# Kernel tuning notes

Hardware: AMD Instinct MI355X
Metric: run time of the kernel (lower is better)

## Reference

```python
import jax, jax.numpy as jnp
import numpy as np

B, IN_DIM, K, OUT_DIM = 512, 16384, 32, 16
DIMS = [8192, 4096, 2048]  # floor(dim/factor) per layer, factor=2


def setup_inputs() -> dict:
    key = jax.random.key(0)
    ks = jax.random.split(key, 16)
    inp = {"x": jax.random.normal(ks[0], (B, IN_DIM), dtype=jnp.float32)}
    prev = IN_DIM
    std = (2.0 / K) ** 0.5
    for i, d in enumerate(DIMS):
        inp[f"w{i}"] = jax.random.normal(ks[1 + i], (d, K), dtype=jnp.float32) * std
        inp[f"b{i}"] = jnp.zeros((1, d), dtype=jnp.float32)
        inp[f"knn{i}"] = jax.random.randint(ks[8 + i], (d, K), 0, prev, dtype=jnp.int64)
        prev = d
    inp["fc_w"] = jax.random.normal(ks[12], (DIMS[-1], OUT_DIM), dtype=jnp.float32) * (1.0 / DIMS[-1] ** 0.5)
    inp["fc_b"] = jnp.zeros((OUT_DIM,), dtype=jnp.float32)
    return inp


def reference(x, w0, b0, w1, b1, w2, b2, fc_w, fc_b, knn0, knn1, knn2):
    # Each layer: gather K neighbors per output unit, weighted sum over K, bias, ReLU.
    for w, b, knn in ((w0, b0, knn0), (w1, b1, knn1), (w2, b2, knn2)):
        g = x[:, knn]                              # (B, dim_i, K) irregular gather
        x = jax.nn.relu(jnp.einsum('bdk,dk->bd', g, w) + b)
    return x @ fc_w + fc_b                         # fc_angle
```

## Files before the change

### kernel.cpp

```cpp
#include <hip/hip_runtime.h>
#include <hip/hip_fp16.h>

#define BATCH   512
#define IN_DIM  16384
#define KNN     32

typedef __attribute__((ext_vector_type(4))) _Float16 half4v;

#define N0 (8192 * KNN)
#define N1 (4096 * KNN)
#define N2 (2048 * KNN)

__global__ __launch_bounds__(256) void prep_k(const int* __restrict__ k0,
                                              const float* __restrict__ w0,
                                              const int* __restrict__ k1,
                                              const float* __restrict__ w1,
                                              const int* __restrict__ k2,
                                              const float* __restrict__ w2,
                                              unsigned int* __restrict__ po) {
    const int t = blockIdx.x * 256 + threadIdx.x;
    int idx; float wv;
    if (t < N0) {
        idx = k0[t];            wv = w0[t];
    } else if (t < N0 + N1) {
        idx = k1[t - N0];       wv = w1[t - N0];
    } else if (t < N0 + N1 + N2) {
        idx = k2[t - N0 - N1];  wv = w2[t - N0 - N1];
    } else {
        return;
    }
    const unsigned short hb =
        __builtin_bit_cast(unsigned short, (_Float16)wv);
    po[t] = (unsigned int)(unsigned short)idx | ((unsigned int)hb << 16);
}

__global__ __launch_bounds__(256) void transpose_h(const float* __restrict__ in,
                                                   _Float16* __restrict__ out) {
    __shared__ float tile[32][33];
    const int bx = blockIdx.x * 32;
    const int by = blockIdx.y * 32;
    const int tx = threadIdx.x & 31;
    const int ty = threadIdx.x >> 5;
#pragma unroll
    for (int j = 0; j < 32; j += 8)
        tile[ty + j][tx] = in[(size_t)(by + ty + j) * IN_DIM + bx + tx];
    __syncthreads();
    const int r = threadIdx.x >> 3;
    const int c = (threadIdx.x & 7) * 4;
    half4v h;
    h[0] = (_Float16)tile[c + 0][r];
    h[1] = (_Float16)tile[c + 1][r];
    h[2] = (_Float16)tile[c + 2][r];
    h[3] = (_Float16)tile[c + 3][r];
    *(half4v*)(out + (size_t)(bx + r) * BATCH + by + c) = h;
}

__global__ __launch_bounds__(256) void lcn_p4(const _Float16* __restrict__ xt,
                                              const unsigned int* __restrict__ packed,
                                              const float* __restrict__ bias,
                                              _Float16* __restrict__ yt) {
    const int lane = threadIdx.x & 63;
    const int wv   = __builtin_amdgcn_readfirstlane(threadIdx.x >> 6);
    const int d    = (blockIdx.x >> 3) * 4 + wv;
    const int b    = (blockIdx.x & 7) * 64 + lane;
    const unsigned int* kp = packed + (size_t)d * KNN;
    const _Float16*     xb = xt + b;
    float acc = 0.f;
#pragma unroll
    for (int k = 0; k < KNN; ++k) {
        const unsigned int u = kp[k];
        const int idx = (int)(u & 0xffffu);
        const _Float16 hw =
            __builtin_bit_cast(_Float16, (unsigned short)(u >> 16));
        acc += (float)hw * (float)xb[(size_t)idx * BATCH];
    }
    acc = fmaxf(acc + bias[d], 0.f);
    yt[(size_t)d * BATCH + b] = (_Float16)acc;
}

__global__ __launch_bounds__(256) void fc_partial(const _Float16* __restrict__ y2t,
                                                  const float* __restrict__ fcw,
                                                  float* __restrict__ part) {
    const int o  = blockIdx.x & 15;
    const int bh = (blockIdx.x >> 4) & 1;
    const int ch = blockIdx.x >> 5;
    const int b  = bh * 256 + threadIdx.x;
    const int d0 = ch * 256;
    float a0 = 0.f, a1 = 0.f, a2 = 0.f, a3 = 0.f;
#pragma unroll 4
    for (int d = d0; d < d0 + 256; d += 4) {
        a0 += (float)y2t[(size_t)(d + 0) * BATCH + b] * fcw[(d + 0) * 16 + o];
        a1 += (float)y2t[(size_t)(d + 1) * BATCH + b] * fcw[(d + 1) * 16 + o];
        a2 += (float)y2t[(size_t)(d + 2) * BATCH + b] * fcw[(d + 2) * 16 + o];
        a3 += (float)y2t[(size_t)(d + 3) * BATCH + b] * fcw[(d + 3) * 16 + o];
    }
    part[((size_t)b * 16 + o) * 8 + ch] = (a0 + a1) + (a2 + a3);
}

__global__ __launch_bounds__(256) void fc_final(const float* __restrict__ part,
                                                const float* __restrict__ fcb,
                                                float* __restrict__ out) {
    const int t = blockIdx.x * 256 + threadIdx.x;
    const float4 p0 = *(const float4*)(part + (size_t)t * 8);
    const float4 p1 = *(const float4*)(part + (size_t)t * 8 + 4);
    out[t] = ((p0.x + p0.y) + (p0.z + p0.w)) + ((p1.x + p1.y) + (p1.z + p1.w))
             + fcb[t & 15];
}

extern "C" void kernel_launch(void* const* d_in, const int* in_sizes, int n_in,
                              void* d_out, int out_size, void* d_ws, size_t ws_size,
                              hipStream_t stream) {
    const float* x    = (const float*)d_in[0];
    const float* w0   = (const float*)d_in[1];
    const float* b0   = (const float*)d_in[2];
    const int*   knn0 = (const int*)  d_in[3];
    const float* w1   = (const float*)d_in[4];
    const float* b1   = (const float*)d_in[5];
    const int*   knn1 = (const int*)  d_in[6];
    const float* w2   = (const float*)d_in[7];
    const float* b2   = (const float*)d_in[8];
    const int*   knn2 = (const int*)  d_in[9];
    const float* fcw  = (const float*)d_in[10];
    const float* fcb  = (const float*)d_in[11];
    float* out = (float*)d_out;

    char* ws = (char*)d_ws;
    _Float16*     xt   = (_Float16*)(ws);
    _Float16*     y0t  = (_Float16*)(ws + ((size_t)16 << 20));
    _Float16*     y1t  = (_Float16*)(ws + ((size_t)24 << 20));
    _Float16*     y2t  = (_Float16*)(ws + ((size_t)28 << 20));
    float*        part = (float*)   (ws + ((size_t)30 << 20));
    unsigned int* po   = (unsigned int*)(ws + ((size_t)30 << 20) + ((size_t)512 << 10));

    prep_k<<<(N0 + N1 + N2 + 255) / 256, 256, 0, stream>>>(knn0, w0, knn1, w1,
                                                           knn2, w2, po);
    transpose_h<<<dim3(IN_DIM / 32, BATCH / 32), 256, 0, stream>>>(x, xt);
    lcn_p4<<<(8192 / 4) * 8, 256, 0, stream>>>(xt,  po,           b0, y0t);
    lcn_p4<<<(4096 / 4) * 8, 256, 0, stream>>>(y0t, po + N0,      b1, y1t);
    lcn_p4<<<(2048 / 4) * 8, 256, 0, stream>>>(y1t, po + N0 + N1, b2, y2t);
    fc_partial<<<256, 256, 0, stream>>>(y2t, fcw, part);
    fc_final<<<32, 256, 0, stream>>>(part, fcb, out);
}
```

Baseline: 70.65 us.

## Bind LCN batch chunks to XCDs via atomic work claiming for L2 locality

Replaces the static grid mapping of the LCN layers with dynamic work claiming. Each block reads its hardware XCD id and atomically takes a slot from a per-XCD chunk counter, so one 64-column batch chunk of the transposed activations tends to stay within one XCD's L2. Each wave now handles several output features in a loop instead of one. The cost is a memset, an atomic per block, and a fallback that steals from other XCDs' counters, which can break the locality when the scheduler spreads blocks unevenly.

```diff
diff --git a/kernel.cpp b/kernel.cpp
--- a/kernel.cpp
+++ b/kernel.cpp
@@ -4,12 +4,20 @@
 #define BATCH   512
 #define IN_DIM  16384
 #define KNN     32
+#define NBLOCKS 2048
+#define SLOTS   256
 
 typedef __attribute__((ext_vector_type(4))) _Float16 half4v;
 
 #define N0 (8192 * KNN)
 #define N1 (4096 * KNN)
 #define N2 (2048 * KNN)
+
+__device__ __forceinline__ int xcd_id() {
+    int x;
+    asm volatile("s_getreg_b32 %0, hwreg(HW_REG_XCC_ID)" : "=s"(x));
+    return x & 7;
+}
 
 __global__ __launch_bounds__(256) void prep_k(const int* __restrict__ k0,
                                               const float* __restrict__ w0,
@@ -29,8 +37,7 @@
     } else {
         return;
     }
-    const unsigned short hb =
-        __builtin_bit_cast(unsigned short, (_Float16)wv);
+    const unsigned short hb = __builtin_bit_cast(unsigned short, (_Float16)wv);
     po[t] = (unsigned int)(unsigned short)idx | ((unsigned int)hb << 16);
 }
 
@@ -55,27 +62,53 @@
     *(half4v*)(out + (size_t)(bx + r) * BATCH + by + c) = h;
 }
 
-__global__ __launch_bounds__(256) void lcn_p4(const _Float16* __restrict__ xt,
+template<int DOUT>
+__global__ __launch_bounds__(256) void lcn_xs(const _Float16* __restrict__ xt,
                                               const unsigned int* __restrict__ packed,
                                               const float* __restrict__ bias,
-                                              _Float16* __restrict__ yt) {
-    const int lane = threadIdx.x & 63;
-    const int wv   = __builtin_amdgcn_readfirstlane(threadIdx.x >> 6);
-    const int d    = (blockIdx.x >> 3) * 4 + wv;
-    const int b    = (blockIdx.x & 7) * 64 + lane;
-    const unsigned int* kp = packed + (size_t)d * KNN;
-    const _Float16*     xb = xt + b;
-    float acc = 0.f;
+                                              _Float16* __restrict__ yt,
+                                              int* __restrict__ ctrs) {
+    constexpr int FPB = DOUT / SLOTS;
+    constexpr int FPW = FPB / 4;
+    __shared__ int s_claim;
+    if (threadIdx.x == 0) {
+        const int x = xcd_id();
+        int claim = -1;
+        for (int q = 0; q < 8; ++q) {
+            const int c = (x + q) & 7;
+            int* p = ctrs + c * 32;
+            if (__hip_atomic_load(p, __ATOMIC_RELAXED,
+                                  __HIP_MEMORY_SCOPE_AGENT) >= SLOTS)
+                continue;
+            const int v = atomicAdd(p, 1);
+            if (v < SLOTS) { claim = (c << 16) | v; break; }
+        }
+        s_claim = claim;
+    }
+    __syncthreads();
+    const int claim = __builtin_amdgcn_readfirstlane(s_claim);
+    if (claim < 0) return;
+    const int chunk = claim >> 16;
+    const int slot  = claim & 0xffff;
+    const int lane  = threadIdx.x & 63;
+    const int wv    = __builtin_amdgcn_readfirstlane(threadIdx.x >> 6);
+    const int b     = chunk * 64 + lane;
+    const _Float16* xb = xt + b;
+    const int dbase = slot * FPB + wv * FPW;
+    for (int i = 0; i < FPW; ++i) {
+        const int d = dbase + i;
+        const unsigned int* kp = packed + (size_t)d * KNN;
+        float acc = 0.f;
 #pragma unroll
-    for (int k = 0; k < KNN; ++k) {
-        const unsigned int u = kp[k];
-        const int idx = (int)(u & 0xffffu);
-        const _Float16 hw =
-            __builtin_bit_cast(_Float16, (unsigned short)(u >> 16));
-        acc += (float)hw * (float)xb[(size_t)idx * BATCH];
+        for (int k = 0; k < KNN; ++k) {
+            const unsigned int u = kp[k];
+            const int idx = (int)(u & 0xffffu);
+            const _Float16 hw =
+                __builtin_bit_cast(_Float16, (unsigned short)(u >> 16));
+            acc += (float)hw * (float)xb[(size_t)idx * BATCH];
+        }
+        yt[(size_t)d * BATCH + b] = (_Float16)fmaxf(acc + bias[d], 0.f);
     }
-    acc = fmaxf(acc + bias[d], 0.f);
-    yt[(size_t)d * BATCH + b] = (_Float16)acc;
 }
 
 __global__ __launch_bounds__(256) void fc_partial(const _Float16* __restrict__ y2t,
@@ -131,13 +164,15 @@
     _Float16*     y2t  = (_Float16*)(ws + ((size_t)28 << 20));
     float*        part = (float*)   (ws + ((size_t)30 << 20));
     unsigned int* po   = (unsigned int*)(ws + ((size_t)30 << 20) + ((size_t)512 << 10));
+    int*          ctrs = (int*)     (ws + ((size_t)33 << 20));
 
+    hipMemsetAsync(ctrs, 0, 3 * 8 * 32 * sizeof(int), stream);
     prep_k<<<(N0 + N1 + N2 + 255) / 256, 256, 0, stream>>>(knn0, w0, knn1, w1,
                                                            knn2, w2, po);
     transpose_h<<<dim3(IN_DIM / 32, BATCH / 32), 256, 0, stream>>>(x, xt);
-    lcn_p4<<<(8192 / 4) * 8, 256, 0, stream>>>(xt,  po,           b0, y0t);
-    lcn_p4<<<(4096 / 4) * 8, 256, 0, stream>>>(y0t, po + N0,      b1, y1t);
-    lcn_p4<<<(2048 / 4) * 8, 256, 0, stream>>>(y1t, po + N0 + N1, b2, y2t);
+    lcn_xs<8192><<<NBLOCKS, 256, 0, stream>>>(xt,  po,           b0, y0t, ctrs);
+    lcn_xs<4096><<<NBLOCKS, 256, 0, stream>>>(y0t, po + N0,      b1, y1t, ctrs + 8 * 32);
+    lcn_xs<2048><<<NBLOCKS, 256, 0, stream>>>(y1t, po + N0 + N1, b2, y2t, ctrs + 16 * 32);
     fc_partial<<<256, 256, 0, stream>>>(y2t, fcw, part);
     fc_final<<<32, 256, 0, stream>>>(part, fcb, out);
 }
```

New measurement: 107.6 us. 52.4% more time.
